# Kernel tuning notes

Measured on AMD Instinct MI355X. Metric: run time of the kernel, lower is better.

Reference implementation:

```python
import jax, jax.numpy as jnp
import numpy as np

TEMPERATURE = 0.07
SIM_THRESHOLD = 0.5


def setup_inputs() -> dict:
    key = jax.random.key(0)
    k1, k2 = jax.random.split(key)
    features = jax.random.normal(k1, (4096, 2, 128), dtype=jnp.float32)
    labels = jax.random.randint(k2, (4096, 100), 0, 2).astype(jnp.float32)
    return {"features": features, "labels": labels}


def reference(features, labels):
    B, V, D = features.shape

    # label Jaccard similarity -> positive/negative masks [B, B]
    intersection = labels @ labels.T
    row_sum = jnp.sum(labels, axis=1, keepdims=True)
    union = row_sum + row_sum.T - intersection
    similarity = intersection / (union + 1e-6)
    positive_mask = (similarity >= SIM_THRESHOLD).astype(jnp.float32)
    negative_mask = 1.0 - positive_mask

    # torch.cat(torch.unbind(features, dim=1), dim=0) -> [V*B, D] (view-major)
    contrast_feature = jnp.transpose(features, (1, 0, 2)).reshape(V * B, D)
    dot_similarities = (contrast_feature @ contrast_feature.T) / TEMPERATURE  # [VB, VB]

    # numerical stability: subtract detached row max over the FULL row
    logits_max = jax.lax.stop_gradient(jnp.max(dot_similarities, axis=1, keepdims=True))
    logits = dot_similarities - logits_max

    # only the top-left [B, B] block is ever indexed by the original loop
    e = jnp.exp(logits[:B, :B])
    pos_sum = jnp.sum(e * positive_mask, axis=1)  # [B]
    neg_sum = jnp.sum(e * negative_mask, axis=1)  # [B]

    has_pos = jnp.sum(positive_mask, axis=1) > 0  # rows with >=1 positive
    pos_safe = jnp.where(has_pos, pos_sum, 1.0)
    den_safe = jnp.where(has_pos, pos_sum + neg_sum, 1.0)
    per_row = -jnp.log(pos_safe / den_safe)

    count = jnp.sum(has_pos.astype(jnp.float32))
    loss = jnp.sum(jnp.where(has_pos, per_row, 0.0)) / jnp.maximum(count, 1.0)
    return loss
```

## Files before the change

### kernel.cpp

```cpp
#include <hip/hip_runtime.h>
#include <math.h>

#define B_ROWS 4096
#define LBL 100
#define NCT 32
#define NTRI 528

typedef __attribute__((ext_vector_type(8))) short bf16x8;
typedef __attribute__((ext_vector_type(4))) float f32x4;

__device__ __forceinline__ unsigned f2bf(float x) {
  union { float f; unsigned u; } a; a.f = x;
  unsigned r = a.u + 0x7fffu + ((a.u >> 16) & 1u);
  return r >> 16;
}
__device__ __forceinline__ float bf2f(unsigned h) {
  return __uint_as_float(h << 16);
}

__global__ void label_kernel(const float* __restrict__ labels,
                             uint4* __restrict__ Lb,
                             int* __restrict__ rsv,
                             float* __restrict__ accum) {
  if (blockIdx.x == 0 && threadIdx.x < 2) accum[threadIdx.x] = 0.0f;
  int w = (int)((blockIdx.x * blockDim.x + threadIdx.x) >> 6);
  int lane = threadIdx.x & 63;
  float x0 = labels[(size_t)w * LBL + lane];
  float x1 = (lane < LBL - 64) ? labels[(size_t)w * LBL + 64 + lane] : 0.0f;
  unsigned long long m0 = __ballot(x0 != 0.0f);
  unsigned long long m1 = __ballot(x1 != 0.0f);
  if (lane == 0) {
    Lb[w] = make_uint4((unsigned)m0, (unsigned)(m0 >> 32),
                       (unsigned)m1, (unsigned)(m1 >> 32));
    rsv[w] = __popcll(m0) + __popcll(m1);
  }
}

__launch_bounds__(256, 2)
__global__ void main_kernel(const float* __restrict__ feat,
                            const uint4* __restrict__ Lb,
                            const int* __restrict__ rsv,
                            float2* __restrict__ part) {
  __shared__ uint4 As[2048];
  __shared__ uint4 Bs[2048];
  __shared__ uint4 rLbS[128], cLbS[128];
  __shared__ int rRsS[128], cRsS[128];
  __shared__ float sS[128], sB[128];

  int bid = blockIdx.x;
  int bx = 0, off = 0;
  while (bid >= off + (NCT - bx)) { off += NCT - bx; ++bx; }
  int by = bx + (bid - off);
  const bool diag = (bx == by);

  const int tid = threadIdx.x;
  const int lane = tid & 63;
  const int l15 = lane & 15;
  const int quad = lane >> 4;
  const int wave = tid >> 6;
  const int wi = (wave & 1) * 64;
  const int wj = (wave >> 1) * 64;
  const int rowBase = bx * 128;
  const int colBase = by * 128;
  const float invT = 1.0f / 0.07f;

  #pragma unroll
  for (int it = 0; it < 8; ++it) {
    int flat = it * 256 + tid;
    int r = flat >> 4, kc = flat & 15;
    const float* pa = feat + (size_t)(rowBase + r) * 256 + kc * 8;
    float4 a0 = *(const float4*)pa;
    float4 a1 = *(const float4*)(pa + 4);
    uint4 av;
    av.x = f2bf(a0.x) | (f2bf(a0.y) << 16);
    av.y = f2bf(a0.z) | (f2bf(a0.w) << 16);
    av.z = f2bf(a1.x) | (f2bf(a1.y) << 16);
    av.w = f2bf(a1.z) | (f2bf(a1.w) << 16);
    As[kc * 128 + (r ^ kc)] = av;
    const float* pb = feat + (size_t)(colBase + r) * 256 + kc * 8;
    float4 b0 = *(const float4*)pb;
    float4 b1 = *(const float4*)(pb + 4);
    uint4 bv;
    bv.x = f2bf(b0.x) | (f2bf(b0.y) << 16);
    bv.y = f2bf(b0.z) | (f2bf(b0.w) << 16);
    bv.z = f2bf(b1.x) | (f2bf(b1.y) << 16);
    bv.w = f2bf(b1.z) | (f2bf(b1.w) << 16);
    Bs[kc * 128 + (r ^ kc)] = bv;
  }
  if (tid < 128) {
    cLbS[tid] = Lb[colBase + tid];
    cRsS[tid] = rsv[colBase + tid];
  } else {
    int t = tid - 128;
    rLbS[t] = Lb[rowBase + t];
    rRsS[t] = rsv[rowBase + t];
  }
  __syncthreads();

  {
    int t = tid & 127;
    const uint4* src = (tid < 128) ? As : Bs;
    float s = 0.f;
    #pragma unroll
    for (int kc = 0; kc < 16; ++kc) {
      uint4 c = src[kc * 128 + (t ^ kc)];
      float v;
      v = bf2f(c.x & 0xffffu); s += v * v;
      v = bf2f(c.x >> 16);     s += v * v;
      v = bf2f(c.y & 0xffffu); s += v * v;
      v = bf2f(c.y >> 16);     s += v * v;
      v = bf2f(c.z & 0xffffu); s += v * v;
      v = bf2f(c.z >> 16);     s += v * v;
      v = bf2f(c.w & 0xffffu); s += v * v;
      v = bf2f(c.w >> 16);     s += v * v;
    }
    if (tid < 128) sS[t] = s - 0.15f;
    else sB[t] = s - 0.15f;
  }
  __syncthreads();

  float srow[16], scol[4];
  #pragma unroll
  for (int ti = 0; ti < 4; ++ti)
    #pragma unroll
    for (int r = 0; r < 4; ++r)
      srow[ti * 4 + r] = sS[wi + ti * 16 + quad * 4 + r];
  #pragma unroll
  for (int tj = 0; tj < 4; ++tj) scol[tj] = sB[wj + tj * 16 + l15];

  const bf16x8* Asv = (const bf16x8*)As;
  const bf16x8* Bsv = (const bf16x8*)Bs;

  f32x4 acc[4][4];
  #pragma unroll
  for (int ti = 0; ti < 4; ++ti)
    #pragma unroll
    for (int tj = 0; tj < 4; ++tj)
      acc[ti][tj] = (f32x4){0.f, 0.f, 0.f, 0.f};

  #pragma unroll
  for (int ks = 0; ks < 4; ++ks) {
    const int kc = ks * 4 + quad;
    const int abase = kc * 128 + wi + (l15 ^ kc);
    const int bbase = kc * 128 + wj + (l15 ^ kc);
    bf16x8 af[4], bfr[4];
    #pragma unroll
    for (int t = 0; t < 4; ++t) {
      af[t] = Asv[abase + t * 16];
      bfr[t] = Bsv[bbase + t * 16];
    }
    #pragma unroll
    for (int ti = 0; ti < 4; ++ti)
      #pragma unroll
      for (int tj = 0; tj < 4; ++tj)
        acc[ti][tj] = __builtin_amdgcn_mfma_f32_16x16x32_bf16(
            af[ti], bfr[tj], acc[ti][tj], 0, 0, 0);
  }

  float p_s[16], n_s[16], cp[4], cn[4], cmax[4];
  #pragma unroll
  for (int i = 0; i < 16; ++i) { p_s[i] = 0.f; n_s[i] = 0.f; }
  #pragma unroll
  for (int tj = 0; tj < 4; ++tj) { cp[tj] = 0.f; cn[tj] = 0.f; cmax[tj] = -1e30f; }

  #pragma unroll
  for (int ti = 0; ti < 4; ++ti)
    #pragma unroll
    for (int r = 0; r < 4; ++r) {
      int si = ti * 4 + r;
      float l0 = acc[ti][0][r], l1 = acc[ti][1][r];
      float l2 = acc[ti][2][r], l3 = acc[ti][3][r];
      cmax[0] = fmaxf(cmax[0], l0);
      cmax[1] = fmaxf(cmax[1], l1);
      cmax[2] = fmaxf(cmax[2], l2);
      cmax[3] = fmaxf(cmax[3], l3);
      float tm = fmaxf(fmaxf(l0, l1), fmaxf(l2, l3));
      if (tm > srow[si] - 6.3f) {
        int lrow = wi + ti * 16 + quad * 4 + r;
        uint4 la = rLbS[lrow];
        int ra = rRsS[lrow];
        float p = p_s[si], n = n_s[si];
        float lv[4] = {l0, l1, l2, l3};
        #pragma unroll
        for (int tj = 0; tj < 4; ++tj) {
          float e = __expf((lv[tj] - srow[si]) * invT);
          int lcol = wj + tj * 16 + l15;
          uint4 lb = cLbS[lcol];
          int inter = __popc(la.x & lb.x) + __popc(la.y & lb.y) +
                      __popc(la.z & lb.z) + __popc(la.w & lb.w);
          if (3 * inter > ra + cRsS[lcol]) p += e; else n += e;
        }
        p_s[si] = p;
        n_s[si] = n;
      }
    }

  if (!diag) {
    #pragma unroll
    for (int tj = 0; tj < 4; ++tj) {
      if (cmax[tj] > scol[tj] - 6.3f) {
        int lcol = wj + tj * 16 + l15;
        uint4 lb = cLbS[lcol];
        int rb = cRsS[lcol];
        float p = cp[tj], n = cn[tj];
        #pragma unroll
        for (int ti = 0; ti < 4; ++ti)
          #pragma unroll
          for (int r = 0; r < 4; ++r) {
            float e = __expf((acc[ti][tj][r] - scol[tj]) * invT);
            int lrow = wi + ti * 16 + quad * 4 + r;
            uint4 la = rLbS[lrow];
            int inter = __popc(la.x & lb.x) + __popc(la.y & lb.y) +
                        __popc(la.z & lb.z) + __popc(la.w & lb.w);
            if (3 * inter > rRsS[lrow] + rb) p += e; else n += e;
          }
        cp[tj] = p;
        cn[tj] = n;
      }
    }
  }

  #pragma unroll
  for (int si = 0; si < 16; ++si) {
    float p = p_s[si], n = n_s[si];
    #pragma unroll
    for (int o = 8; o >= 1; o >>= 1) {
      p += __shfl_xor(p, o);
      n += __shfl_xor(n, o);
    }
    p_s[si] = p;
    n_s[si] = n;
  }
  #pragma unroll
  for (int tj = 0; tj < 4; ++tj) {
    float p = cp[tj], n = cn[tj];
    p += __shfl_xor(p, 16); n += __shfl_xor(n, 16);
    p += __shfl_xor(p, 32); n += __shfl_xor(n, 32);
    cp[tj] = p;
    cn[tj] = n;
  }

  __syncthreads();
  float* mrow = (float*)As;
  float* mcol = ((float*)As) + 256;
  if (wj == 64 && l15 == 0) {
    #pragma unroll
    for (int ti = 0; ti < 4; ++ti)
      #pragma unroll
      for (int r = 0; r < 4; ++r) {
        int row = wi + ti * 16 + quad * 4 + r;
        int si = ti * 4 + r;
        mrow[row * 2 + 0] = p_s[si];
        mrow[row * 2 + 1] = n_s[si];
      }
  }
  if (!diag && wi == 64 && quad == 0) {
    #pragma unroll
    for (int tj = 0; tj < 4; ++tj) {
      int col = wj + tj * 16 + l15;
      mcol[col * 2 + 0] = cp[tj];
      mcol[col * 2 + 1] = cn[tj];
    }
  }
  __syncthreads();
  if (wj == 0 && l15 == 0) {
    #pragma unroll
    for (int ti = 0; ti < 4; ++ti)
      #pragma unroll
      for (int r = 0; r < 4; ++r) {
        int row = wi + ti * 16 + quad * 4 + r;
        int si = ti * 4 + r;
        float p = p_s[si] + mrow[row * 2 + 0];
        float n = n_s[si] + mrow[row * 2 + 1];
        part[(size_t)by * B_ROWS + rowBase + row] = make_float2(p, n);
      }
  }
  if (!diag && wi == 0 && quad == 0) {
    #pragma unroll
    for (int tj = 0; tj < 4; ++tj) {
      int col = wj + tj * 16 + l15;
      float p = cp[tj] + mcol[col * 2 + 0];
      float n = cn[tj] + mcol[col * 2 + 1];
      part[(size_t)bx * B_ROWS + colBase + col] = make_float2(p, n);
    }
  }
}

__global__ void merge_kernel(const float2* __restrict__ part,
                             const int* __restrict__ rsv,
                             float* __restrict__ accum) {
  int row = blockIdx.x * 256 + threadIdx.x;
  float p = 0.f, n = 0.f;
  #pragma unroll
  for (int c = 0; c < NCT; ++c) {
    float2 v = part[(size_t)c * B_ROWS + row];
    p += v.x;
    n += v.y;
  }
  float per = 0.f, cnt = 0.f;
  if (rsv[row] > 0) {
    per = -logf(p / (p + n));
    cnt = 1.f;
  }
  #pragma unroll
  for (int o = 32; o >= 1; o >>= 1) {
    per += __shfl_xor(per, o);
    cnt += __shfl_xor(cnt, o);
  }
  if ((threadIdx.x & 63) == 0) {
    atomicAdd(accum + 0, per);
    atomicAdd(accum + 1, cnt);
  }
}

__global__ void fin_kernel(const float* __restrict__ accum,
                           float* __restrict__ out) {
  out[0] = accum[0] / fmaxf(accum[1], 1.0f);
}

extern "C" void kernel_launch(void* const* d_in, const int* in_sizes, int n_in,
                              void* d_out, int out_size, void* d_ws, size_t ws_size,
                              hipStream_t stream) {
  const float* feat = (const float*)d_in[0];
  const float* labels = (const float*)d_in[1];
  float* out = (float*)d_out;
  char* ws = (char*)d_ws;
  uint4* Lbm = (uint4*)(ws + 0);
  int* rsv = (int*)(ws + 65536);
  float2* part = (float2*)(ws + 81920);
  float* accum = (float*)(ws + 81920 + 1048576);

  hipLaunchKernelGGL(label_kernel, dim3(1024), dim3(256), 0, stream,
                     labels, Lbm, rsv, accum);
  hipLaunchKernelGGL(main_kernel, dim3(NTRI), dim3(256), 0, stream,
                     feat, Lbm, rsv, part);
  hipLaunchKernelGGL(merge_kernel, dim3(B_ROWS / 256), dim3(256), 0, stream,
                     part, rsv, accum);
  hipLaunchKernelGGL(fin_kernel, dim3(1), dim3(1), 0, stream, accum, out);
}
```

Baseline: 82.94 us.

## Replace symmetric triangular tiling with full tile grid and fuse merge/finalize

Drops the upper-triangle tile scheme that exploited symmetry of the feature Gram matrix. Every 128x128 tile is now computed independently over a 32x32 grid, and each block produces only row partials. This removes the column-side exp/popcount pass, its shuffles and shared-memory exchange, and the triangular index search, at the cost of nearly doubling the MFMA and tile-load work. The merge and finalize kernels are fused into a single-block kernel with no atomics, which cuts one launch but serialises the reduction of 4096 rows in one block.

```diff
diff --git a/kernel.cpp b/kernel.cpp
--- a/kernel.cpp
+++ b/kernel.cpp
@@ -4,7 +4,6 @@
 #define B_ROWS 4096
 #define LBL 100
 #define NCT 32
-#define NTRI 528
 
 typedef __attribute__((ext_vector_type(8))) short bf16x8;
 typedef __attribute__((ext_vector_type(4))) float f32x4;
@@ -20,9 +19,7 @@
 
 __global__ void label_kernel(const float* __restrict__ labels,
                              uint4* __restrict__ Lb,
-                             int* __restrict__ rsv,
-                             float* __restrict__ accum) {
-  if (blockIdx.x == 0 && threadIdx.x < 2) accum[threadIdx.x] = 0.0f;
+                             int* __restrict__ rsv) {
   int w = (int)((blockIdx.x * blockDim.x + threadIdx.x) >> 6);
   int lane = threadIdx.x & 63;
   float x0 = labels[(size_t)w * LBL + lane];
@@ -45,14 +42,10 @@
   __shared__ uint4 Bs[2048];
   __shared__ uint4 rLbS[128], cLbS[128];
   __shared__ int rRsS[128], cRsS[128];
-  __shared__ float sS[128], sB[128];
-
-  int bid = blockIdx.x;
-  int bx = 0, off = 0;
-  while (bid >= off + (NCT - bx)) { off += NCT - bx; ++bx; }
-  int by = bx + (bid - off);
-  const bool diag = (bx == by);
-
+  __shared__ float sS[128];
+
+  const int bx = blockIdx.x;
+  const int by = blockIdx.y;
   const int tid = threadIdx.x;
   const int lane = tid & 63;
   const int l15 = lane & 15;
@@ -97,13 +90,11 @@
   }
   __syncthreads();
 
-  {
-    int t = tid & 127;
-    const uint4* src = (tid < 128) ? As : Bs;
+  if (tid < 128) {
     float s = 0.f;
     #pragma unroll
     for (int kc = 0; kc < 16; ++kc) {
-      uint4 c = src[kc * 128 + (t ^ kc)];
+      uint4 c = As[kc * 128 + (tid ^ kc)];
       float v;
       v = bf2f(c.x & 0xffffu); s += v * v;
       v = bf2f(c.x >> 16);     s += v * v;
@@ -114,19 +105,16 @@
       v = bf2f(c.w & 0xffffu); s += v * v;
       v = bf2f(c.w >> 16);     s += v * v;
     }
-    if (tid < 128) sS[t] = s - 0.15f;
-    else sB[t] = s - 0.15f;
-  }
-  __syncthreads();
-
-  float srow[16], scol[4];
+    sS[tid] = s - 0.15f;
+  }
+  __syncthreads();
+
+  float srow[16];
   #pragma unroll
   for (int ti = 0; ti < 4; ++ti)
     #pragma unroll
     for (int r = 0; r < 4; ++r)
       srow[ti * 4 + r] = sS[wi + ti * 16 + quad * 4 + r];
-  #pragma unroll
-  for (int tj = 0; tj < 4; ++tj) scol[tj] = sB[wj + tj * 16 + l15];
 
   const bf16x8* Asv = (const bf16x8*)As;
   const bf16x8* Bsv = (const bf16x8*)Bs;
@@ -157,12 +145,9 @@
             af[ti], bfr[tj], acc[ti][tj], 0, 0, 0);
   }
 
-  float p_s[16], n_s[16], cp[4], cn[4], cmax[4];
+  float p_s[16], n_s[16];
   #pragma unroll
   for (int i = 0; i < 16; ++i) { p_s[i] = 0.f; n_s[i] = 0.f; }
-  #pragma unroll
-  for (int tj = 0; tj < 4; ++tj) { cp[tj] = 0.f; cn[tj] = 0.f; cmax[tj] = -1e30f; }
-
   #pragma unroll
   for (int ti = 0; ti < 4; ++ti)
     #pragma unroll
@@ -170,10 +155,6 @@
       int si = ti * 4 + r;
       float l0 = acc[ti][0][r], l1 = acc[ti][1][r];
       float l2 = acc[ti][2][r], l3 = acc[ti][3][r];
-      cmax[0] = fmaxf(cmax[0], l0);
-      cmax[1] = fmaxf(cmax[1], l1);
-      cmax[2] = fmaxf(cmax[2], l2);
-      cmax[3] = fmaxf(cmax[3], l3);
       float tm = fmaxf(fmaxf(l0, l1), fmaxf(l2, l3));
       if (tm > srow[si] - 6.3f) {
         int lrow = wi + ti * 16 + quad * 4 + r;
@@ -195,31 +176,6 @@
       }
     }
 
-  if (!diag) {
-    #pragma unroll
-    for (int tj = 0; tj < 4; ++tj) {
-      if (cmax[tj] > scol[tj] - 6.3f) {
-        int lcol = wj + tj * 16 + l15;
-        uint4 lb = cLbS[lcol];
-        int rb = cRsS[lcol];
-        float p = cp[tj], n = cn[tj];
-        #pragma unroll
-        for (int ti = 0; ti < 4; ++ti)
-          #pragma unroll
-          for (int r = 0; r < 4; ++r) {
-            float e = __expf((acc[ti][tj][r] - scol[tj]) * invT);
-            int lrow = wi + ti * 16 + quad * 4 + r;
-            uint4 la = rLbS[lrow];
-            int inter = __popc(la.x & lb.x) + __popc(la.y & lb.y) +
-                        __popc(la.z & lb.z) + __popc(la.w & lb.w);
-            if (3 * inter > rRsS[lrow] + rb) p += e; else n += e;
-          }
-        cp[tj] = p;
-        cn[tj] = n;
-      }
-    }
-  }
-
   #pragma unroll
   for (int si = 0; si < 16; ++si) {
     float p = p_s[si], n = n_s[si];
@@ -231,18 +187,9 @@
     p_s[si] = p;
     n_s[si] = n;
   }
-  #pragma unroll
-  for (int tj = 0; tj < 4; ++tj) {
-    float p = cp[tj], n = cn[tj];
-    p += __shfl_xor(p, 16); n += __shfl_xor(n, 16);
-    p += __shfl_xor(p, 32); n += __shfl_xor(n, 32);
-    cp[tj] = p;
-    cn[tj] = n;
-  }
-
-  __syncthreads();
-  float* mrow = (float*)As;
-  float* mcol = ((float*)As) + 256;
+
+  __syncthreads();
+  float* mbuf = (float*)As;
   if (wj == 64 && l15 == 0) {
     #pragma unroll
     for (int ti = 0; ti < 4; ++ti)
@@ -250,17 +197,9 @@
       for (int r = 0; r < 4; ++r) {
         int row = wi + ti * 16 + quad * 4 + r;
         int si = ti * 4 + r;
-        mrow[row * 2 + 0] = p_s[si];
-        mrow[row * 2 + 1] = n_s[si];
+        mbuf[row * 2 + 0] = p_s[si];
+        mbuf[row * 2 + 1] = n_s[si];
       }
-  }
-  if (!diag && wi == 64 && quad == 0) {
-    #pragma unroll
-    for (int tj = 0; tj < 4; ++tj) {
-      int col = wj + tj * 16 + l15;
-      mcol[col * 2 + 0] = cp[tj];
-      mcol[col * 2 + 1] = cn[tj];
-    }
   }
   __syncthreads();
   if (wj == 0 && l15 == 0) {
@@ -270,52 +209,47 @@
       for (int r = 0; r < 4; ++r) {
         int row = wi + ti * 16 + quad * 4 + r;
         int si = ti * 4 + r;
-        float p = p_s[si] + mrow[row * 2 + 0];
-        float n = n_s[si] + mrow[row * 2 + 1];
+        float p = p_s[si] + mbuf[row * 2 + 0];
+        float n = n_s[si] + mbuf[row * 2 + 1];
         part[(size_t)by * B_ROWS + rowBase + row] = make_float2(p, n);
       }
   }
-  if (!diag && wi == 0 && quad == 0) {
-    #pragma unroll
-    for (int tj = 0; tj < 4; ++tj) {
-      int col = wj + tj * 16 + l15;
-      float p = cp[tj] + mcol[col * 2 + 0];
-      float n = cn[tj] + mcol[col * 2 + 1];
-      part[(size_t)bx * B_ROWS + colBase + col] = make_float2(p, n);
-    }
-  }
-}
-
-__global__ void merge_kernel(const float2* __restrict__ part,
-                             const int* __restrict__ rsv,
-                             float* __restrict__ accum) {
-  int row = blockIdx.x * 256 + threadIdx.x;
-  float p = 0.f, n = 0.f;
-  #pragma unroll
-  for (int c = 0; c < NCT; ++c) {
-    float2 v = part[(size_t)c * B_ROWS + row];
-    p += v.x;
-    n += v.y;
-  }
+}
+
+__global__ void mergefin_kernel(const float2* __restrict__ part,
+                                const int* __restrict__ rsv,
+                                float* __restrict__ out) {
+  __shared__ float red[8];
+  int t = threadIdx.x;
   float per = 0.f, cnt = 0.f;
-  if (rsv[row] > 0) {
-    per = -logf(p / (p + n));
-    cnt = 1.f;
+  #pragma unroll
+  for (int i = 0; i < 16; ++i) {
+    int row = i * 256 + t;
+    float p = 0.f, n = 0.f;
+    #pragma unroll
+    for (int c = 0; c < NCT; ++c) {
+      float2 v = part[(size_t)c * B_ROWS + row];
+      p += v.x;
+      n += v.y;
+    }
+    if (rsv[row] > 0) {
+      per += -logf(p / (p + n));
+      cnt += 1.f;
+    }
   }
   #pragma unroll
   for (int o = 32; o >= 1; o >>= 1) {
     per += __shfl_xor(per, o);
     cnt += __shfl_xor(cnt, o);
   }
-  if ((threadIdx.x & 63) == 0) {
-    atomicAdd(accum + 0, per);
-    atomicAdd(accum + 1, cnt);
-  }
-}
-
-__global__ void fin_kernel(const float* __restrict__ accum,
-                           float* __restrict__ out) {
-  out[0] = accum[0] / fmaxf(accum[1], 1.0f);
+  int wv = t >> 6;
+  if ((t & 63) == 0) { red[wv * 2] = per; red[wv * 2 + 1] = cnt; }
+  __syncthreads();
+  if (t == 0) {
+    float P = red[0] + red[2] + red[4] + red[6];
+    float C = red[1] + red[3] + red[5] + red[7];
+    out[0] = P / fmaxf(C, 1.0f);
+  }
 }
 
 extern "C" void kernel_launch(void* const* d_in, const int* in_sizes, int n_in,
@@ -328,13 +262,11 @@
   uint4* Lbm = (uint4*)(ws + 0);
   int* rsv = (int*)(ws + 65536);
   float2* part = (float2*)(ws + 81920);
-  float* accum = (float*)(ws + 81920 + 1048576);
 
   hipLaunchKernelGGL(label_kernel, dim3(1024), dim3(256), 0, stream,
-                     labels, Lbm, rsv, accum);
-  hipLaunchKernelGGL(main_kernel, dim3(NTRI), dim3(256), 0, stream,
+                     labels, Lbm, rsv);
+  hipLaunchKernelGGL(main_kernel, dim3(NCT, NCT), dim3(256), 0, stream,
                      feat, Lbm, rsv, part);
-  hipLaunchKernelGGL(merge_kernel, dim3(B_ROWS / 256), dim3(256), 0, stream,
-                     part, rsv, accum);
-  hipLaunchKernelGGL(fin_kernel, dim3(1), dim3(1), 0, stream, accum, out);
-}
+  hipLaunchKernelGGL(mergefin_kernel, dim3(1), dim3(256), 0, stream,
+                     part, rsv, out);
+}
```

After: 105.5 us. +27.2%, slower.

## Pre-pack features to swizzled bf16 and load tiles via global-to-LDS DMA

Applied to the files above, without the earlier changes.

Adds a pack kernel that converts the fp32 features once into a bf16, XOR-swizzled tile layout in workspace. The main kernel then fills its shared-memory tiles with direct global-to-LDS loads instead of converting per tile, roughly halving tile load bytes. Row squared norms are computed once in the label kernel rather than per tile from LDS, which removes one barrier. The cost is an extra kernel launch and an extra pass over the features.

```diff
diff --git a/kernel.cpp b/kernel.cpp
--- a/kernel.cpp
+++ b/kernel.cpp
@@ -14,17 +14,45 @@
   unsigned r = a.u + 0x7fffu + ((a.u >> 16) & 1u);
   return r >> 16;
 }
-__device__ __forceinline__ float bf2f(unsigned h) {
-  return __uint_as_float(h << 16);
-}
-
-__global__ void label_kernel(const float* __restrict__ labels,
-                             uint4* __restrict__ Lb,
-                             int* __restrict__ rsv,
-                             float* __restrict__ accum) {
+
+__device__ __forceinline__ void lds_dma16(void* l, const void* g) {
+  __builtin_amdgcn_global_load_lds(
+      (const __attribute__((address_space(1))) void*)g,
+      (__attribute__((address_space(3))) void*)l, 16, 0, 0);
+}
+
+__global__ void pack_kernel(const float* __restrict__ feat,
+                            uint4* __restrict__ cf) {
+  int g = blockIdx.x * 256 + threadIdx.x;
+  int tile = g >> 11, rem = g & 2047;
+  int r = rem >> 4, kc = rem & 15;
+  const float* src = feat + ((size_t)(tile * 128 + r)) * 256 + kc * 8;
+  float4 a = *(const float4*)src;
+  float4 b = *(const float4*)(src + 4);
+  uint4 ov;
+  ov.x = f2bf(a.x) | (f2bf(a.y) << 16);
+  ov.y = f2bf(a.z) | (f2bf(a.w) << 16);
+  ov.z = f2bf(b.x) | (f2bf(b.y) << 16);
+  ov.w = f2bf(b.z) | (f2bf(b.w) << 16);
+  cf[(size_t)tile * 2048 + kc * 128 + (r ^ kc)] = ov;
+}
+
+__global__ void seedlabel_kernel(const float* __restrict__ feat,
+                                 const float* __restrict__ labels,
+                                 uint4* __restrict__ Lb,
+                                 int* __restrict__ rsv,
+                                 float* __restrict__ seedRaw,
+                                 float* __restrict__ accum) {
   if (blockIdx.x == 0 && threadIdx.x < 2) accum[threadIdx.x] = 0.0f;
   int w = (int)((blockIdx.x * blockDim.x + threadIdx.x) >> 6);
   int lane = threadIdx.x & 63;
+  const float2* src = (const float2*)(feat + (size_t)w * 256);
+  float2 f = src[lane];
+  float b0 = __uint_as_float(f2bf(f.x) << 16);
+  float b1 = __uint_as_float(f2bf(f.y) << 16);
+  float s = b0 * b0 + b1 * b1;
+  #pragma unroll
+  for (int o = 32; o >= 1; o >>= 1) s += __shfl_xor(s, o);
   float x0 = labels[(size_t)w * LBL + lane];
   float x1 = (lane < LBL - 64) ? labels[(size_t)w * LBL + 64 + lane] : 0.0f;
   unsigned long long m0 = __ballot(x0 != 0.0f);
@@ -33,13 +61,15 @@
     Lb[w] = make_uint4((unsigned)m0, (unsigned)(m0 >> 32),
                        (unsigned)m1, (unsigned)(m1 >> 32));
     rsv[w] = __popcll(m0) + __popcll(m1);
+    seedRaw[w] = s - 0.15f;
   }
 }
 
 __launch_bounds__(256, 2)
-__global__ void main_kernel(const float* __restrict__ feat,
+__global__ void main_kernel(const uint4* __restrict__ cf,
                             const uint4* __restrict__ Lb,
                             const int* __restrict__ rsv,
+                            const float* __restrict__ seedRaw,
                             float2* __restrict__ part) {
   __shared__ uint4 As[2048];
   __shared__ uint4 Bs[2048];
@@ -67,55 +97,18 @@
   #pragma unroll
   for (int it = 0; it < 8; ++it) {
     int flat = it * 256 + tid;
-    int r = flat >> 4, kc = flat & 15;
-    const float* pa = feat + (size_t)(rowBase + r) * 256 + kc * 8;
-    float4 a0 = *(const float4*)pa;
-    float4 a1 = *(const float4*)(pa + 4);
-    uint4 av;
-    av.x = f2bf(a0.x) | (f2bf(a0.y) << 16);
-    av.y = f2bf(a0.z) | (f2bf(a0.w) << 16);
-    av.z = f2bf(a1.x) | (f2bf(a1.y) << 16);
-    av.w = f2bf(a1.z) | (f2bf(a1.w) << 16);
-    As[kc * 128 + (r ^ kc)] = av;
-    const float* pb = feat + (size_t)(colBase + r) * 256 + kc * 8;
-    float4 b0 = *(const float4*)pb;
-    float4 b1 = *(const float4*)(pb + 4);
-    uint4 bv;
-    bv.x = f2bf(b0.x) | (f2bf(b0.y) << 16);
-    bv.y = f2bf(b0.z) | (f2bf(b0.w) << 16);
-    bv.z = f2bf(b1.x) | (f2bf(b1.y) << 16);
-    bv.w = f2bf(b1.z) | (f2bf(b1.w) << 16);
-    Bs[kc * 128 + (r ^ kc)] = bv;
+    lds_dma16(&As[flat], &cf[(size_t)bx * 2048 + flat]);
+    lds_dma16(&Bs[flat], &cf[(size_t)by * 2048 + flat]);
   }
   if (tid < 128) {
     cLbS[tid] = Lb[colBase + tid];
     cRsS[tid] = rsv[colBase + tid];
+    sB[tid] = seedRaw[colBase + tid];
   } else {
     int t = tid - 128;
     rLbS[t] = Lb[rowBase + t];
     rRsS[t] = rsv[rowBase + t];
-  }
-  __syncthreads();
-
-  {
-    int t = tid & 127;
-    const uint4* src = (tid < 128) ? As : Bs;
-    float s = 0.f;
-    #pragma unroll
-    for (int kc = 0; kc < 16; ++kc) {
-      uint4 c = src[kc * 128 + (t ^ kc)];
-      float v;
-      v = bf2f(c.x & 0xffffu); s += v * v;
-      v = bf2f(c.x >> 16);     s += v * v;
-      v = bf2f(c.y & 0xffffu); s += v * v;
-      v = bf2f(c.y >> 16);     s += v * v;
-      v = bf2f(c.z & 0xffffu); s += v * v;
-      v = bf2f(c.z >> 16);     s += v * v;
-      v = bf2f(c.w & 0xffffu); s += v * v;
-      v = bf2f(c.w >> 16);     s += v * v;
-    }
-    if (tid < 128) sS[t] = s - 0.15f;
-    else sB[t] = s - 0.15f;
+    sS[t] = seedRaw[rowBase + t];
   }
   __syncthreads();
 
@@ -325,15 +318,18 @@
   const float* labels = (const float*)d_in[1];
   float* out = (float*)d_out;
   char* ws = (char*)d_ws;
-  uint4* Lbm = (uint4*)(ws + 0);
-  int* rsv = (int*)(ws + 65536);
-  float2* part = (float2*)(ws + 81920);
-  float* accum = (float*)(ws + 81920 + 1048576);
-
-  hipLaunchKernelGGL(label_kernel, dim3(1024), dim3(256), 0, stream,
-                     labels, Lbm, rsv, accum);
+  uint4* cf = (uint4*)(ws + 0);
+  uint4* Lbm = (uint4*)(ws + 1048576);
+  int* rsv = (int*)(ws + 1114112);
+  float* seedRaw = (float*)(ws + 1130496);
+  float2* part = (float2*)(ws + 1146880);
+  float* accum = (float*)(ws + 1146880 + 1048576);
+
+  hipLaunchKernelGGL(pack_kernel, dim3(256), dim3(256), 0, stream, feat, cf);
+  hipLaunchKernelGGL(seedlabel_kernel, dim3(1024), dim3(256), 0, stream,
+                     feat, labels, Lbm, rsv, seedRaw, accum);
   hipLaunchKernelGGL(main_kernel, dim3(NTRI), dim3(256), 0, stream,
-                     feat, Lbm, rsv, part);
+                     cf, Lbm, rsv, seedRaw, part);
   hipLaunchKernelGGL(merge_kernel, dim3(B_ROWS / 256), dim3(256), 0, stream,
                      part, rsv, accum);
   hipLaunchKernelGGL(fin_kernel, dim3(1), dim3(1), 0, stream, accum, out);
```

Result: no change. 83.31 us (+0.4%).
